# Kernel tuning notes

Hardware: AMD Instinct MI355X
Metric: run time of the kernel (lower is better)

## Reference

```python
import jax, jax.numpy as jnp
import numpy as np

B = 256        # number of graphs
NPG = 256      # nodes per graph
N = B * NPG    # total nodes
F = 128        # node feature dim
DEG = 16       # avg degree
E = N * DEG    # total edges
LAT = [32, 32, 32, 1]
D = sum(LAT)   # total_latent_dim = 97
K = 30         # sortpool k
C1, C2, KW2 = 16, 32, 5
DENSE = ((K - 2) // 2 + 1 - KW2 + 1) * C2  # 352
OUT = 2


def setup_inputs() -> dict:
    key = jax.random.key(0)
    ks = jax.random.split(key, 16)
    node_feat = jax.random.normal(ks[0], (N, F), jnp.float32)
    # edges constrained within each graph (block-diagonal adjacency)
    base = ((jnp.arange(E, dtype=jnp.int32) // (E // B)) * NPG).astype(jnp.int32)
    src = jax.random.randint(ks[1], (E,), 0, NPG, dtype=jnp.int32) + base
    dst = jax.random.randint(ks[2], (E,), 0, NPG, dtype=jnp.int32) + base
    degs = jnp.zeros((N,), jnp.int32).at[dst].add(1)  # in-degree per node
    s = 0.1
    dims = [F] + LAT
    inp = {"node_feat": node_feat, "src": src, "dst": dst, "degs": degs}
    for i in range(4):
        inp[f"W{i}"] = jax.random.normal(ks[3 + i], (dims[i], dims[i + 1]), jnp.float32) * s
        inp[f"b{i}"] = jnp.zeros((dims[i + 1],), jnp.float32)
    inp["conv1_w"] = jax.random.normal(ks[8], (C1, 1, D), jnp.float32) * s
    inp["conv1_b"] = jnp.zeros((C1,), jnp.float32)
    inp["conv2_w"] = jax.random.normal(ks[9], (C2, C1, KW2), jnp.float32) * s
    inp["conv2_b"] = jnp.zeros((C2,), jnp.float32)
    inp["out_w"] = jax.random.normal(ks[10], (DENSE, OUT), jnp.float32) * s
    inp["out_b"] = jnp.zeros((OUT,), jnp.float32)
    return inp


def reference(node_feat, W0, b0, W1, b1, W2, b2, W3, b3,
              conv1_w, conv1_b, conv2_w, conv2_b, out_w, out_b,
              src, dst, degs):
    n = node_feat.shape[0]
    deg1 = (degs.astype(node_feat.dtype) + 1.0)[:, None]  # node_degs = deg + 1
    h = node_feat
    feats = []
    for W, b in ((W0, b0), (W1, b1), (W2, b2), (W3, b3)):
        # gnn_spmm(n2n, h) + h : sparse adjacency matmul via segment add
        pooled = jnp.zeros((n, h.shape[1]), h.dtype).at[dst].add(h[src]) + h
        h = jnp.tanh((pooled @ W + b) / deg1)
        feats.append(h)
    Z = jnp.concatenate(feats, axis=1)          # [N, D]
    Zb = Z.reshape(B, NPG, D)                   # equal-sized graphs
    # sortpooling: top-k on last latent channel per graph, gather rows
    _, idx = jax.lax.top_k(Zb[:, :, -1], K)     # [B, K]
    sp = jnp.take_along_axis(Zb, idx[:, :, None], axis=1)  # [B, K, D]
    x = sp.reshape(B, 1, K * D)
    dn = ('NCH', 'OIH', 'NCH')
    x = jax.lax.conv_general_dilated(x, conv1_w, (D,), 'VALID', dimension_numbers=dn)
    x = jax.nn.relu(x + conv1_b[None, :, None])          # [B, C1, K]
    x = x.reshape(B, C1, K // 2, 2).max(axis=-1)         # maxpool1d(2,2) -> [B, C1, 15]
    x = jax.lax.conv_general_dilated(x, conv2_w, (1,), 'VALID', dimension_numbers=dn)
    x = jax.nn.relu(x + conv2_b[None, :, None])          # [B, C2, 11]
    to_dense = x.reshape(B, -1)                          # [B, 352]
    out = jax.nn.relu(to_dense @ out_w + out_b)
    return jax.nn.relu(out)  # original applies conv1d_activation twice at the end
```

## Files before the change

### kernel.cpp

```cpp
#include <hip/hip_runtime.h>

#define NPG  256
#define EPG  4096
#define FDIM 128
#define KTOP 30

__global__ __launch_bounds__(256, 1)
void dgcnn_fused(const float* __restrict__ node_feat,
                 const int* __restrict__ srcv, const int* __restrict__ dstv,
                 const int* __restrict__ degs,
                 const float* __restrict__ W0, const float* __restrict__ b0,
                 const float* __restrict__ W1, const float* __restrict__ b1,
                 const float* __restrict__ W2, const float* __restrict__ b2,
                 const float* __restrict__ W3, const float* __restrict__ b3,
                 const float* __restrict__ cw1, const float* __restrict__ cb1,
                 const float* __restrict__ cw2, const float* __restrict__ cb2,
                 const float* __restrict__ ow,  const float* __restrict__ ob,
                 float* __restrict__ outp)
{
    __shared__ float Ybuf[NPG * 33];
    __shared__ int   srclist[EPG];
    __shared__ int   offs[NPG];
    __shared__ int   cnt [NPG];
    __shared__ int   degl[NPG];
    __shared__ float invd[NPG];
    __shared__ float keys[NPG];
    __shared__ int   sel [KTOP + 2];

    const int g = blockIdx.x;
    const int t = threadIdx.x;

    int dn = degs[g * NPG + t];
    degl[t] = dn;
    cnt[t]  = 0;
    invd[t] = 1.0f / (float)(dn + 1);
    offs[t] = dn;
    __syncthreads();
    for (int s = 1; s < NPG; s <<= 1) {
        int v = (t >= s) ? offs[t - s] : 0;
        __syncthreads();
        offs[t] += v;
        __syncthreads();
    }
    int excl = offs[t] - dn;
    __syncthreads();
    offs[t] = excl;
    __syncthreads();
    {
        const int* sg = srcv + g * EPG;
        const int* dg = dstv + g * EPG;
        for (int i = 0; i < EPG / NPG; i++) {
            int e  = t + i * NPG;
            int ss = sg[e] & (NPG - 1);
            int dd = dg[e] & (NPG - 1);
            int p  = atomicAdd(&cnt[dd], 1);
            srclist[offs[dd] + p] = ss;
        }
    }

    float acc[32];
    #pragma unroll
    for (int c = 0; c < 32; c++) acc[c] = 0.f;
    {
        const float* nf = node_feat + (size_t)g * NPG * FDIM;
        for (int kc = 0; kc < 4; kc++) {
            __syncthreads();
            #pragma unroll
            for (int i = 0; i < 8; i++) {
                int Fi = t + i * 256;
                int n  = Fi >> 3, k4 = Fi & 7;
                const float4 v = *(const float4*)(nf + n * FDIM + kc * 32 + k4 * 4);
                float* p = &Ybuf[n * 33 + k4 * 4];
                p[0] = v.x; p[1] = v.y; p[2] = v.z; p[3] = v.w;
            }
            __syncthreads();
            #pragma unroll
            for (int k = 0; k < 32; k++) {
                float h = Ybuf[t * 33 + k];
                const float* wr = W0 + (kc * 32 + k) * 32;
                #pragma unroll
                for (int c = 0; c < 32; c++) acc[c] = fmaf(h, wr[c], acc[c]);
            }
        }
        __syncthreads();
        #pragma unroll
        for (int c = 0; c < 32; c++) Ybuf[t * 33 + c] = acc[c];
        __syncthreads();
    }

    float h1[32], h2[32], h3[32];
    const float iv = invd[t];
    const int   o  = offs[t];
    const int   d  = degl[t];

    auto agg = [&](float (&h)[32]) {
        #pragma unroll
        for (int c = 0; c < 32; c++) h[c] = Ybuf[t * 33 + c];
        for (int j = 0; j < d; j++) {
            int a = srclist[o + j];
            const float* yr = &Ybuf[a * 33];
            #pragma unroll
            for (int c = 0; c < 32; c++) h[c] += yr[c];
        }
    };
    auto act = [&](float (&h)[32], const float* bb) {
        #pragma unroll
        for (int c = 0; c < 32; c++) h[c] = tanhf((h[c] + bb[c]) * iv);
    };
    auto matml = [&](const float (&h)[32], const float* Wn) {
        float a[32];
        #pragma unroll
        for (int c = 0; c < 32; c++) a[c] = 0.f;
        #pragma unroll
        for (int k = 0; k < 32; k++) {
            const float* wr = Wn + k * 32;
            float hk = h[k];
            #pragma unroll
            for (int c = 0; c < 32; c++) a[c] = fmaf(hk, wr[c], a[c]);
        }
        __syncthreads();
        #pragma unroll
        for (int c = 0; c < 32; c++) Ybuf[t * 33 + c] = a[c];
        __syncthreads();
    };

    agg(h1); act(h1, b0); matml(h1, W1);
    agg(h2); act(h2, b1); matml(h2, W2);
    agg(h3); act(h3, b2);
    {
        float a3 = 0.f;
        #pragma unroll
        for (int k = 0; k < 32; k++) a3 = fmaf(h3[k], W3[k], a3);
        __syncthreads();
        Ybuf[t * 33] = a3;
        __syncthreads();
    }
    float kv;
    {
        float s = Ybuf[t * 33];
        for (int j = 0; j < d; j++) s += Ybuf[srclist[o + j] * 33];
        kv = tanhf((s + b3[0]) * iv);
        keys[t] = kv;
    }
    __syncthreads();

    int rank = 0;
    #pragma unroll 4
    for (int j = 0; j < NPG; j++) {
        float vj = keys[j];
        rank += ((vj > kv) || ((vj == kv) && (j < t))) ? 1 : 0;
    }
    if (rank < KTOP) sel[rank] = t;
    __syncthreads();

    float* sp    = (float*)srclist;
    float* x1    = sp + 30 * 97;
    float* xp    = x1 + 480;
    float* dense = xp + 240;

    if (rank < KTOP) {
        float* dp = sp + rank * 97;
        #pragma unroll
        for (int c = 0; c < 32; c++) dp[c]      = h1[c];
        #pragma unroll
        for (int c = 0; c < 32; c++) dp[32 + c] = h2[c];
        #pragma unroll
        for (int c = 0; c < 32; c++) dp[64 + c] = h3[c];
        dp[96] = kv;
    }
    __syncthreads();

    for (int idx = t; idx < 480; idx += 256) {
        int k = idx >> 4, c = idx & 15;
        float s = cb1[c];
        for (int dd = 0; dd < 97; dd++) s = fmaf(sp[k * 97 + dd], cw1[c * 97 + dd], s);
        x1[c * 30 + k] = fmaxf(s, 0.f);
    }
    __syncthreads();
    for (int idx = t; idx < 240; idx += 256) {
        int c = idx / 15, k = idx - c * 15;
        xp[idx] = fmaxf(x1[c * 30 + 2 * k], x1[c * 30 + 2 * k + 1]);
    }
    __syncthreads();
    for (int idx = t; idx < 352; idx += 256) {
        int c = idx / 11, j = idx - c * 11;
        float s = cb2[c];
        for (int i2 = 0; i2 < 16; i2++) {
            #pragma unroll
            for (int tt = 0; tt < 5; tt++)
                s = fmaf(xp[i2 * 15 + j + tt], cw2[(c * 16 + i2) * 5 + tt], s);
        }
        dense[idx] = fmaxf(s, 0.f);
    }
    __syncthreads();
    if (t < 64) {
        float a0 = 0.f, a1 = 0.f;
        for (int dd = t; dd < 352; dd += 64) {
            float v = dense[dd];
            a0 = fmaf(v, ow[dd * 2],     a0);
            a1 = fmaf(v, ow[dd * 2 + 1], a1);
        }
        #pragma unroll
        for (int off2 = 32; off2 > 0; off2 >>= 1) {
            a0 += __shfl_down(a0, off2);
            a1 += __shfl_down(a1, off2);
        }
        if (t == 0) {
            outp[g * 2 + 0] = fmaxf(a0 + ob[0], 0.f);
            outp[g * 2 + 1] = fmaxf(a1 + ob[1], 0.f);
        }
    }
}

extern "C" void kernel_launch(void* const* d_in, const int* in_sizes, int n_in,
                              void* d_out, int out_size, void* d_ws, size_t ws_size,
                              hipStream_t stream) {
    const float* node_feat = (const float*)d_in[0];
    const int*   src       = (const int*)  d_in[1];
    const int*   dst       = (const int*)  d_in[2];
    const int*   degsp     = (const int*)  d_in[3];
    const float* W0 = (const float*)d_in[4];
    const float* b0 = (const float*)d_in[5];
    const float* W1 = (const float*)d_in[6];
    const float* b1 = (const float*)d_in[7];
    const float* W2 = (const float*)d_in[8];
    const float* b2 = (const float*)d_in[9];
    const float* W3 = (const float*)d_in[10];
    const float* b3 = (const float*)d_in[11];
    const float* cw1 = (const float*)d_in[12];
    const float* cb1 = (const float*)d_in[13];
    const float* cw2 = (const float*)d_in[14];
    const float* cb2 = (const float*)d_in[15];
    const float* ow  = (const float*)d_in[16];
    const float* ob  = (const float*)d_in[17];

    dgcnn_fused<<<dim3(256), dim3(256), 0, stream>>>(
        node_feat, src, dst, degsp,
        W0, b0, W1, b1, W2, b2, W3, b3,
        cw1, cb1, cw2, cb2, ow, ob, (float*)d_out);
}
```

Before: 181.8 us.

## Use wave-shuffle scan, direct per-thread W0 matmul, sorted neighbor lists, unrolled aggregation

Replaces the shared-memory Hillis-Steele degree scan with a wave-level shuffle scan plus a cross-wave fixup. The first-layer matmul no longer stages node features through LDS; each thread reads its own row directly with float4 loads, double-buffered in registers. Each thread insertion-sorts its neighbor list so that deterministic float addition order is kept, and the aggregation loops are unrolled by four to expose more independent LDS loads. The unused sel array and one barrier are removed. The direct row reads are strided across threads, which may hurt coalescing, and the serial per-thread sort adds work.

```diff
diff --git a/kernel.cpp b/kernel.cpp
--- a/kernel.cpp
+++ b/kernel.cpp
@@ -25,30 +25,37 @@
     __shared__ int   degl[NPG];
     __shared__ float invd[NPG];
     __shared__ float keys[NPG];
-    __shared__ int   sel [KTOP + 2];
+    __shared__ int   wsum[4];
 
     const int g = blockIdx.x;
     const int t = threadIdx.x;
 
-    int dn = degs[g * NPG + t];
+    const int dn = degs[g * NPG + t];
     degl[t] = dn;
     cnt[t]  = 0;
     invd[t] = 1.0f / (float)(dn + 1);
-    offs[t] = dn;
-    __syncthreads();
-    for (int s = 1; s < NPG; s <<= 1) {
-        int v = (t >= s) ? offs[t - s] : 0;
-        __syncthreads();
-        offs[t] += v;
-        __syncthreads();
-    }
-    int excl = offs[t] - dn;
-    __syncthreads();
-    offs[t] = excl;
-    __syncthreads();
+    {
+        int v = dn;
+        const int lane = t & 63;
+        #pragma unroll
+        for (int off = 1; off < 64; off <<= 1) {
+            int u = __shfl_up(v, off);
+            if (lane >= off) v += u;
+        }
+        if (lane == 63) wsum[t >> 6] = v;
+        __syncthreads();
+        const int w = t >> 6;
+        int base = 0;
+        #pragma unroll
+        for (int i = 0; i < 4; i++) base += (i < w) ? wsum[i] : 0;
+        offs[t] = base + v - dn;
+        __syncthreads();
+    }
+
     {
         const int* sg = srcv + g * EPG;
         const int* dg = dstv + g * EPG;
+        #pragma unroll
         for (int i = 0; i < EPG / NPG; i++) {
             int e  = t + i * NPG;
             int ss = sg[e] & (NPG - 1);
@@ -57,48 +64,91 @@
             srclist[offs[dd] + p] = ss;
         }
     }
-
-    float acc[32];
-    #pragma unroll
-    for (int c = 0; c < 32; c++) acc[c] = 0.f;
-    {
-        const float* nf = node_feat + (size_t)g * NPG * FDIM;
-        for (int kc = 0; kc < 4; kc++) {
-            __syncthreads();
-            #pragma unroll
-            for (int i = 0; i < 8; i++) {
-                int Fi = t + i * 256;
-                int n  = Fi >> 3, k4 = Fi & 7;
-                const float4 v = *(const float4*)(nf + n * FDIM + kc * 32 + k4 * 4);
-                float* p = &Ybuf[n * 33 + k4 * 4];
-                p[0] = v.x; p[1] = v.y; p[2] = v.z; p[3] = v.w;
-            }
-            __syncthreads();
-            #pragma unroll
-            for (int k = 0; k < 32; k++) {
-                float h = Ybuf[t * 33 + k];
-                const float* wr = W0 + (kc * 32 + k) * 32;
-                #pragma unroll
-                for (int c = 0; c < 32; c++) acc[c] = fmaf(h, wr[c], acc[c]);
-            }
-        }
-        __syncthreads();
-        #pragma unroll
-        for (int c = 0; c < 32; c++) Ybuf[t * 33 + c] = acc[c];
-        __syncthreads();
-    }
-
-    float h1[32], h2[32], h3[32];
+    __syncthreads();
+
     const float iv = invd[t];
     const int   o  = offs[t];
     const int   d  = degl[t];
 
+    for (int i = 1; i < d; i++) {
+        int key = srclist[o + i];
+        int j = i - 1;
+        while (j >= 0 && srclist[o + j] > key) {
+            srclist[o + j + 1] = srclist[o + j];
+            --j;
+        }
+        srclist[o + j + 1] = key;
+    }
+
+    {
+        const float4* nf4 = (const float4*)(node_feat + ((size_t)g * NPG + t) * FDIM);
+        float acc[32];
+        #pragma unroll
+        for (int c = 0; c < 32; c++) acc[c] = 0.f;
+
+        auto fma4 = [&](float4 r, int kbase) {
+            const float* w0 = W0 + (kbase + 0) * 32;
+            const float* w1 = W0 + (kbase + 1) * 32;
+            const float* w2 = W0 + (kbase + 2) * 32;
+            const float* w3 = W0 + (kbase + 3) * 32;
+            #pragma unroll
+            for (int c = 0; c < 32; c++) {
+                float a = acc[c];
+                a = fmaf(r.x, w0[c], a);
+                a = fmaf(r.y, w1[c], a);
+                a = fmaf(r.z, w2[c], a);
+                a = fmaf(r.w, w3[c], a);
+                acc[c] = a;
+            }
+        };
+
+        float4 A0 = nf4[0], A1 = nf4[1], A2 = nf4[2], A3 = nf4[3];
+        float4 B0 = nf4[4], B1 = nf4[5], B2 = nf4[6], B3 = nf4[7];
+        fma4(A0,   0); fma4(A1,   4); fma4(A2,   8); fma4(A3,  12);
+        A0 = nf4[8];  A1 = nf4[9];  A2 = nf4[10]; A3 = nf4[11];
+        fma4(B0,  16); fma4(B1,  20); fma4(B2,  24); fma4(B3,  28);
+        B0 = nf4[12]; B1 = nf4[13]; B2 = nf4[14]; B3 = nf4[15];
+        fma4(A0,  32); fma4(A1,  36); fma4(A2,  40); fma4(A3,  44);
+        A0 = nf4[16]; A1 = nf4[17]; A2 = nf4[18]; A3 = nf4[19];
+        fma4(B0,  48); fma4(B1,  52); fma4(B2,  56); fma4(B3,  60);
+        B0 = nf4[20]; B1 = nf4[21]; B2 = nf4[22]; B3 = nf4[23];
+        fma4(A0,  64); fma4(A1,  68); fma4(A2,  72); fma4(A3,  76);
+        A0 = nf4[24]; A1 = nf4[25]; A2 = nf4[26]; A3 = nf4[27];
+        fma4(B0,  80); fma4(B1,  84); fma4(B2,  88); fma4(B3,  92);
+        B0 = nf4[28]; B1 = nf4[29]; B2 = nf4[30]; B3 = nf4[31];
+        fma4(A0,  96); fma4(A1, 100); fma4(A2, 104); fma4(A3, 108);
+        fma4(B0, 112); fma4(B1, 116); fma4(B2, 120); fma4(B3, 124);
+
+        #pragma unroll
+        for (int c = 0; c < 32; c++) Ybuf[t * 33 + c] = acc[c];
+        __syncthreads();
+    }
+
     auto agg = [&](float (&h)[32]) {
-        #pragma unroll
-        for (int c = 0; c < 32; c++) h[c] = Ybuf[t * 33 + c];
-        for (int j = 0; j < d; j++) {
-            int a = srclist[o + j];
-            const float* yr = &Ybuf[a * 33];
+        const float* self = &Ybuf[t * 33];
+        #pragma unroll
+        for (int c = 0; c < 32; c++) h[c] = self[c];
+        int j = 0;
+        for (; j + 4 <= d; j += 4) {
+            const int a0 = srclist[o + j + 0];
+            const int a1 = srclist[o + j + 1];
+            const int a2 = srclist[o + j + 2];
+            const int a3 = srclist[o + j + 3];
+            const float* r0 = &Ybuf[a0 * 33];
+            const float* r1 = &Ybuf[a1 * 33];
+            const float* r2 = &Ybuf[a2 * 33];
+            const float* r3 = &Ybuf[a3 * 33];
+            #pragma unroll
+            for (int c = 0; c < 32; c++) h[c] += r0[c];
+            #pragma unroll
+            for (int c = 0; c < 32; c++) h[c] += r1[c];
+            #pragma unroll
+            for (int c = 0; c < 32; c++) h[c] += r2[c];
+            #pragma unroll
+            for (int c = 0; c < 32; c++) h[c] += r3[c];
+        }
+        for (; j < d; j++) {
+            const float* yr = &Ybuf[srclist[o + j] * 33];
             #pragma unroll
             for (int c = 0; c < 32; c++) h[c] += yr[c];
         }
@@ -114,7 +164,7 @@
         #pragma unroll
         for (int k = 0; k < 32; k++) {
             const float* wr = Wn + k * 32;
-            float hk = h[k];
+            const float  hk = h[k];
             #pragma unroll
             for (int c = 0; c < 32; c++) a[c] = fmaf(hk, wr[c], a[c]);
         }
@@ -124,6 +174,7 @@
         __syncthreads();
     };
 
+    float h1[32], h2[32], h3[32];
     agg(h1); act(h1, b0); matml(h1, W1);
     agg(h2); act(h2, b1); matml(h2, W2);
     agg(h3); act(h3, b2);
@@ -138,7 +189,18 @@
     float kv;
     {
         float s = Ybuf[t * 33];
-        for (int j = 0; j < d; j++) s += Ybuf[srclist[o + j] * 33];
+        int j = 0;
+        for (; j + 4 <= d; j += 4) {
+            const int a0 = srclist[o + j + 0];
+            const int a1 = srclist[o + j + 1];
+            const int a2 = srclist[o + j + 2];
+            const int a3i = srclist[o + j + 3];
+            s += Ybuf[a0 * 33];
+            s += Ybuf[a1 * 33];
+            s += Ybuf[a2 * 33];
+            s += Ybuf[a3i * 33];
+        }
+        for (; j < d; j++) s += Ybuf[srclist[o + j] * 33];
         kv = tanhf((s + b3[0]) * iv);
         keys[t] = kv;
     }
@@ -150,8 +212,6 @@
         float vj = keys[j];
         rank += ((vj > kv) || ((vj == kv) && (j < t))) ? 1 : 0;
     }
-    if (rank < KTOP) sel[rank] = t;
-    __syncthreads();
 
     float* sp    = (float*)srclist;
     float* x1    = sp + 30 * 97;
```

After: 305.8 us. 68.2% more time.
